# Kernel tuning notes

Measured on AMD Instinct MI355X. Metric: run time of the kernel, lower is better.

The kernel has to match this reference:

```python
import jax, jax.numpy as jnp
import numpy as np

DIM = 1024
NUM_HEADS = 16
HEAD_DIM = DIM // NUM_HEADS
SCALE = HEAD_DIM ** -0.5


def setup_inputs() -> dict:
    key = jax.random.key(0)
    ks = jax.random.split(key, 6)
    B, N, C = 2, 2048, DIM
    std = 1.0 / np.sqrt(C)
    x = jax.random.normal(ks[0], (B, N, C), dtype=jnp.float32)
    wq = jax.random.normal(ks[1], (C, C), dtype=jnp.float32) * std
    wk = jax.random.normal(ks[2], (C, C), dtype=jnp.float32) * std
    wv = jax.random.normal(ks[3], (C, C), dtype=jnp.float32) * std
    w_proj = jax.random.normal(ks[4], (C, C), dtype=jnp.float32) * std
    b_proj = jax.random.normal(ks[5], (C,), dtype=jnp.float32) * 0.01
    return {"x": x, "wq": wq, "wk": wk, "wv": wv, "w_proj": w_proj, "b_proj": b_proj}


def reference(x, wq, wk, wv, w_proj, b_proj):
    B, N, C = x.shape
    H, D = NUM_HEADS, HEAD_DIM
    Nq = N // 2
    # q from first half of tokens; k, v from all tokens
    q = (x[:, :Nq] @ wq.T).reshape(B, Nq, H, D).transpose(0, 2, 1, 3)  # [B,H,Nq,D]
    k = (x @ wk.T).reshape(B, N, H, D).transpose(0, 2, 1, 3)           # [B,H,N,D]
    v = (x @ wv.T).reshape(B, N, H, D).transpose(0, 2, 1, 3)           # [B,H,N,D]
    attn = jnp.einsum('bhqd,bhkd->bhqk', q, k) * SCALE
    attn = jax.nn.softmax(attn, axis=-1)
    out = jnp.einsum('bhqk,bhkd->bhqd', attn, v)                       # [B,H,Nq,D]
    out = out.transpose(0, 2, 1, 3).reshape(B, Nq, C)
    return out @ w_proj.T + b_proj
```

## Files before the change

### kernel.cpp

```cpp
#include <hip/hip_runtime.h>

typedef _Float16 f16;
typedef _Float16 f16x8 __attribute__((ext_vector_type(8)));
typedef _Float16 f16x4 __attribute__((ext_vector_type(4)));
typedef float f32x4 __attribute__((ext_vector_type(4)));

#define MFMA_F16(a, b, c) __builtin_amdgcn_mfma_f32_16x16x32_f16(a, b, c, 0, 0, 0)

__device__ __forceinline__ void gld16(const void* g, void* l) {
  __builtin_amdgcn_global_load_lds(
      (const __attribute__((address_space(1))) unsigned int*)(unsigned long long)g,
      (__attribute__((address_space(3))) unsigned int*)(unsigned long long)l, 16, 0, 0);
}

__global__ __launch_bounds__(256) void cvt_x_kernel(const float* __restrict__ in,
                                                    f16* __restrict__ out, int n8) {
  int i = blockIdx.x * 256 + threadIdx.x;
  if (i >= n8) return;
  const float4* p = (const float4*)(in + (size_t)i * 8);
  float4 a = p[0], b = p[1];
  f16x8 o = {(f16)a.x, (f16)a.y, (f16)a.z, (f16)a.w,
             (f16)b.x, (f16)b.y, (f16)b.z, (f16)b.w};
  *(f16x8*)(out + (size_t)i * 8) = o;
}

__global__ __launch_bounds__(256) void cvt_w4_kernel(const float* __restrict__ w0,
                                                     const float* __restrict__ w1,
                                                     const float* __restrict__ w2,
                                                     const float* __restrict__ w3,
                                                     f16* __restrict__ out) {
  int i = blockIdx.x * 256 + threadIdx.x;
  int t = i >> 17, r = i & 131071;
  const float* w = (t == 0) ? w0 : (t == 1) ? w1 : (t == 2) ? w2 : w3;
  const float4* p = (const float4*)(w + (size_t)r * 8);
  float4 a = p[0], b = p[1];
  f16x8 o = {(f16)a.x, (f16)a.y, (f16)a.z, (f16)a.w,
             (f16)b.x, (f16)b.y, (f16)b.z, (f16)b.w};
  *(f16x8*)(out + (size_t)t * 1048576 + (size_t)r * 8) = o;
}

__global__ __launch_bounds__(256) void qkv_gemm_kernel(
    const f16* __restrict__ A, const f16* __restrict__ Wq,
    const f16* __restrict__ Wk, const f16* __restrict__ Wv,
    f16* __restrict__ Qo, f16* __restrict__ Ko, f16* __restrict__ Vo) {
  __shared__ __align__(16) f16 As[128 * 64];
  __shared__ __align__(16) f16 Bs[128 * 64];
  const int y = blockIdx.y;
  const f16* Bw;
  f16* Co;
  int mt;
  if (y < 16) { Bw = Wq; Co = Qo; mt = (y & 7) | ((y >> 3) << 4); }
  else if (y < 48) { Bw = Wk; Co = Ko; mt = y - 16; }
  else { Bw = Wv; Co = Vo; mt = y - 48; }
  const int m0 = mt * 128, n0 = blockIdx.x * 128;
  const int tid = threadIdx.x, lane = tid & 63, w = tid >> 6;
  const int wr = w >> 1, wc = w & 1, g = lane >> 4, c = lane & 15;
  const int r_st = tid >> 3, t_st = tid & 7;

  f32x4 acc[4][4] = {};

  for (int k0 = 0; k0 < 1024; k0 += 64) {
#pragma unroll
    for (int i = 0; i < 4; ++i) {
      int row = r_st + i * 32;
      int sl = (t_st ^ (row & 7)) * 8;
      gld16(&A[(size_t)(m0 + row) * 1024 + k0 + sl], &As[(row * 8 + t_st) * 8]);
      gld16(&Bw[(size_t)(n0 + row) * 1024 + k0 + sl], &Bs[(row * 8 + t_st) * 8]);
    }
    __syncthreads();
#pragma unroll
    for (int kb = 0; kb < 2; ++kb) {
      f16x8 af[4], bf[4];
#pragma unroll
      for (int m2 = 0; m2 < 4; ++m2)
        af[m2] = *(const f16x8*)&As[(wr * 64 + m2 * 16 + c) * 64 +
                                    (((kb * 4 + g) ^ (c & 7)) * 8)];
#pragma unroll
      for (int nt = 0; nt < 4; ++nt)
        bf[nt] = *(const f16x8*)&Bs[(wc * 64 + nt * 16 + c) * 64 +
                                    (((kb * 4 + g) ^ (c & 7)) * 8)];
#pragma unroll
      for (int m2 = 0; m2 < 4; ++m2)
#pragma unroll
        for (int nt = 0; nt < 4; ++nt)
          acc[m2][nt] = MFMA_F16(af[m2], bf[nt], acc[m2][nt]);
    }
    __syncthreads();
  }

#pragma unroll
  for (int m2 = 0; m2 < 4; ++m2)
#pragma unroll
    for (int nt = 0; nt < 4; ++nt) {
      int col = n0 + wc * 64 + nt * 16 + c;
#pragma unroll
      for (int r = 0; r < 4; ++r)
        Co[(size_t)(m0 + wr * 64 + m2 * 16 + g * 4 + r) * 1024 + col] =
            (f16)acc[m2][nt][r];
    }
}

__global__ __launch_bounds__(256) void proj_gemm_kernel(
    const f16* __restrict__ A, const f16* __restrict__ Bw,
    float* __restrict__ C, const float* __restrict__ bias) {
  __shared__ __align__(16) f16 As[64 * 64];
  __shared__ __align__(16) f16 Bs[128 * 64];
  const int m0 = blockIdx.y * 64, n0 = blockIdx.x * 128;
  const int tid = threadIdx.x, lane = tid & 63, w = tid >> 6;
  const int wr = w >> 1, wc = w & 1, g = lane >> 4, c = lane & 15;
  const int r_st = tid >> 3, t_st = tid & 7;

  f32x4 acc[2][4] = {};

  for (int k0 = 0; k0 < 1024; k0 += 64) {
#pragma unroll
    for (int i = 0; i < 2; ++i) {
      int row = r_st + i * 32;
      int sl = (t_st ^ (row & 7)) * 8;
      gld16(&A[(size_t)(m0 + row) * 1024 + k0 + sl], &As[(row * 8 + t_st) * 8]);
    }
#pragma unroll
    for (int i = 0; i < 4; ++i) {
      int row = r_st + i * 32;
      int sl = (t_st ^ (row & 7)) * 8;
      gld16(&Bw[(size_t)(n0 + row) * 1024 + k0 + sl], &Bs[(row * 8 + t_st) * 8]);
    }
    __syncthreads();
#pragma unroll
    for (int kb = 0; kb < 2; ++kb) {
      f16x8 af[2], bf[4];
#pragma unroll
      for (int m2 = 0; m2 < 2; ++m2)
        af[m2] = *(const f16x8*)&As[(wr * 32 + m2 * 16 + c) * 64 +
                                    (((kb * 4 + g) ^ (c & 7)) * 8)];
#pragma unroll
      for (int nt = 0; nt < 4; ++nt)
        bf[nt] = *(const f16x8*)&Bs[(wc * 64 + nt * 16 + c) * 64 +
                                    (((kb * 4 + g) ^ (c & 7)) * 8)];
#pragma unroll
      for (int m2 = 0; m2 < 2; ++m2)
#pragma unroll
        for (int nt = 0; nt < 4; ++nt)
          acc[m2][nt] = MFMA_F16(af[m2], bf[nt], acc[m2][nt]);
    }
    __syncthreads();
  }

#pragma unroll
  for (int m2 = 0; m2 < 2; ++m2)
#pragma unroll
    for (int nt = 0; nt < 4; ++nt) {
      int col = n0 + wc * 64 + nt * 16 + c;
      float bv = bias[col];
#pragma unroll
      for (int r = 0; r < 4; ++r)
        C[(size_t)(m0 + wr * 32 + m2 * 16 + g * 4 + r) * 1024 + col] =
            acc[m2][nt][r] + bv;
    }
}

__global__ __launch_bounds__(256) void transpose_v_kernel(const f16* __restrict__ V,
                                                          f16* __restrict__ VT) {
  const int LDT = 72;
  __shared__ __align__(16) f16 T[64 * 72];
  const int n0 = blockIdx.x * 64, h = blockIdx.y, b = blockIdx.z;
  const int tid = threadIdx.x;
#pragma unroll
  for (int i = 0; i < 2; ++i) {
    int idx = tid + i * 256;
    int row = idx >> 3, c8 = idx & 7;
    *(f16x8*)&T[row * LDT + c8 * 8] =
        *(const f16x8*)&V[(size_t)(b * 2048 + n0 + row) * 1024 + h * 64 + c8 * 8];
  }
  __syncthreads();
#pragma unroll
  for (int i = 0; i < 2; ++i) {
    int idx = tid + i * 256;
    int d = idx >> 3, c8 = idx & 7;
    f16x8 v;
#pragma unroll
    for (int j = 0; j < 8; ++j) v[j] = T[(c8 * 8 + j) * LDT + d];
    *(f16x8*)&VT[((size_t)((b * 16 + h) * 64 + d)) * 2048 + n0 + c8 * 8] = v;
  }
}

__global__ __launch_bounds__(256, 4) void attn_kernel(const f16* __restrict__ Q,
                                                      const f16* __restrict__ Kg,
                                                      const f16* __restrict__ VT,
                                                      f16* __restrict__ Opart,
                                                      float2* __restrict__ ML) {
  __shared__ __align__(16) f16 Ks[2][64 * 64];
  __shared__ __align__(16) f16 Vs[2][64 * 64];
  __shared__ __align__(16) f16 Ps[4][16 * 64];
  const int qt = blockIdx.x, h = blockIdx.y;
  const int b = blockIdx.z >> 1, ch = blockIdx.z & 1;
  const int tid = threadIdx.x, lane = tid & 63, w = tid >> 6;
  const int g = lane >> 4, c = lane & 15;
  const int r_st = tid >> 3, t_st = tid & 7;

  const f16* Kbase = Kg + (size_t)(b * 2048 + ch * 1024) * 1024 + h * 64;
  const f16* Vbase = VT + ((size_t)((b * 16 + h) * 64)) * 2048 + ch * 1024;

  f16x8 qf[2];
  {
    const f16* qp = Q + (size_t)(b * 2048 + qt * 64 + w * 16 + c) * 1024 + h * 64;
    qf[0] = *(const f16x8*)(qp + g * 8);
    qf[1] = *(const f16x8*)(qp + 32 + g * 8);
#pragma unroll
    for (int j = 0; j < 8; ++j) {
      qf[0][j] = (f16)((float)qf[0][j] * 0.1803368801f);
      qf[1][j] = (f16)((float)qf[1][j] * 0.1803368801f);
    }
  }

  auto stage = [&](int t, int buf) {
#pragma unroll
    for (int i = 0; i < 2; ++i) {
      int row = r_st + i * 32;
      int sl = (t_st ^ (row & 7)) * 8;
      gld16(&Kbase[(size_t)(t * 64 + row) * 1024 + sl],
            &Ks[buf][(row * 8 + t_st) * 8]);
      gld16(&Vbase[(size_t)row * 2048 + t * 64 + sl],
            &Vs[buf][(row * 8 + t_st) * 8]);
    }
  };

  f32x4 oacc[4] = {};
  float l_run = 0.f;

  stage(0, 0);
  __syncthreads();

  for (int t = 0; t < 16; ++t) {
    const int cur = t & 1;
    if (t < 15) stage(t + 1, cur ^ 1);

    f32x4 s[4] = {};
#pragma unroll
    for (int kt = 0; kt < 4; ++kt) {
      f16x8 kf0 = *(const f16x8*)&Ks[cur][(kt * 16 + c) * 64 + ((g ^ (c & 7)) * 8)];
      f16x8 kf1 =
          *(const f16x8*)&Ks[cur][(kt * 16 + c) * 64 + (((4 + g) ^ (c & 7)) * 8)];
      s[kt] = MFMA_F16(kf0, qf[0], s[kt]);
      s[kt] = MFMA_F16(kf1, qf[1], s[kt]);
    }

    float rsum = 0.f;
#pragma unroll
    for (int kt = 0; kt < 4; ++kt)
#pragma unroll
      for (int r = 0; r < 4; ++r) {
        float p = exp2f(s[kt][r]);
        s[kt][r] = p;
        rsum += p;
      }
    rsum += __shfl_xor(rsum, 16);
    rsum += __shfl_xor(rsum, 32);
    l_run += rsum;

#pragma unroll
    for (int kt = 0; kt < 4; ++kt) {
      f16x4 pv = {(f16)s[kt][0], (f16)s[kt][1], (f16)s[kt][2], (f16)s[kt][3]};
      *(f16x4*)&Ps[w][c * 64 + (((kt * 2 + (g >> 1)) ^ (c & 7)) * 8) + (g & 1) * 4] =
          pv;
    }

#pragma unroll
    for (int kb = 0; kb < 2; ++kb) {
      f16x8 pf =
          *(const f16x8*)&Ps[w][c * 64 + (((kb * 4 + g) ^ (c & 7)) * 8)];
#pragma unroll
      for (int dt = 0; dt < 4; ++dt) {
        f16x8 vf = *(const f16x8*)&Vs[cur][(dt * 16 + c) * 64 +
                                           (((kb * 4 + g) ^ (c & 7)) * 8)];
        oacc[dt] = MFMA_F16(pf, vf, oacc[dt]);
      }
    }

    __syncthreads();
  }

  float li[4];
#pragma unroll
  for (int r = 0; r < 4; ++r) li[r] = 1.f / __shfl(l_run, g * 4 + r);
#pragma unroll
  for (int dt = 0; dt < 4; ++dt)
#pragma unroll
    for (int r = 0; r < 4; ++r) {
      Opart[(size_t)ch * 2097152 +
            (size_t)(b * 1024 + qt * 64 + w * 16 + g * 4 + r) * 1024 + h * 64 +
            dt * 16 + c] = (f16)(oacc[dt][r] * li[r]);
    }
  if (lane < 16)
    ML[ch * 32768 + (b * 1024 + qt * 64 + w * 16 + lane) * 16 + h] =
        make_float2(0.f, l_run);
}

__global__ __launch_bounds__(256) void combine_kernel(const f16* __restrict__ Opart,
                                                      const float2* __restrict__ ML,
                                                      f16* __restrict__ O16) {
  int i = blockIdx.x * 256 + threadIdx.x;
  int row = i >> 7;
  int h = (i & 127) >> 3;
  float2 a = ML[row * 16 + h];
  float2 bml = ML[32768 + row * 16 + h];
  float m = fmaxf(a.x, bml.x);
  float w0 = exp2f(a.x - m) * a.y;
  float w1 = exp2f(bml.x - m) * bml.y;
  float inv = 1.f / (w0 + w1);
  float a0 = w0 * inv, a1 = w1 * inv;
  f16x8 o0 = *(const f16x8*)&Opart[(size_t)i * 8];
  f16x8 o1 = *(const f16x8*)&Opart[2097152 + (size_t)i * 8];
  f16x8 r;
#pragma unroll
  for (int j = 0; j < 8; ++j) r[j] = (f16)(a0 * (float)o0[j] + a1 * (float)o1[j]);
  *(f16x8*)&O16[(size_t)i * 8] = r;
}

extern "C" void kernel_launch(void* const* d_in, const int* in_sizes, int n_in,
                              void* d_out, int out_size, void* d_ws, size_t ws_size,
                              hipStream_t stream) {
  const float* x = (const float*)d_in[0];
  const float* wq = (const float*)d_in[1];
  const float* wk = (const float*)d_in[2];
  const float* wv = (const float*)d_in[3];
  const float* wp = (const float*)d_in[4];
  const float* bp = (const float*)d_in[5];
  float* out = (float*)d_out;

  char* p = (char*)d_ws;
  f16* x16 = (f16*)p;  p += (size_t)4194304 * 2;
  f16* w16 = (f16*)p;  p += (size_t)4 * 1048576 * 2;
  f16* Q16 = (f16*)p;  p += (size_t)4194304 * 2;
  f16* K16 = (f16*)p;  p += (size_t)4194304 * 2;
  f16* V16 = (f16*)p;  p += (size_t)4194304 * 2;
  f16* VT16 = (f16*)p; p += (size_t)4194304 * 2;
  f16* O16 = (f16*)p;  p += (size_t)2097152 * 2;

  f16* wq16 = w16;
  f16* wk16 = w16 + 1048576;
  f16* wv16 = w16 + 2 * 1048576;
  f16* wp16 = w16 + 3 * 1048576;

  cvt_x_kernel<<<4194304 / 8 / 256, 256, 0, stream>>>(x, x16, 4194304 / 8);
  cvt_w4_kernel<<<4 * 131072 / 256, 256, 0, stream>>>(wq, wk, wv, wp, w16);

  qkv_gemm_kernel<<<dim3(8, 80), 256, 0, stream>>>(x16, wq16, wk16, wv16, Q16, K16,
                                                   V16);

  transpose_v_kernel<<<dim3(32, 16, 2), 256, 0, stream>>>(V16, VT16);

  f16* Opart = V16;
  float2* MLp = (float2*)x16;
  attn_kernel<<<dim3(16, 16, 4), 256, 0, stream>>>(Q16, K16, VT16, Opart, MLp);
  combine_kernel<<<1024, 256, 0, stream>>>(Opart, MLp, O16);

  proj_gemm_kernel<<<dim3(8, 32), 256, 0, stream>>>(O16, wp16, out, bp);
}
```

Baseline: 114.5 us.

## Double-buffer GEMMs, fuse V transpose into QKV epilogue, swizzle block order

The QKV and projection GEMMs now double-buffer their shared-memory tiles, issuing the next k-tile's async global-to-LDS loads before computing on the current one. The QKV epilogue writes V directly in transposed layout, so the separate transpose kernel and its extra round trip through global memory are removed. Block indices in the GEMMs and the attention kernel are remapped with an XCD-style swizzle to improve L2 locality across chiplets. The projection GEMM moves to 64x64 tiles with twice as many blocks, and LDS use per block doubles in the QKV GEMM, which may lower occupancy.

```diff
diff --git a/kernel.cpp b/kernel.cpp
--- a/kernel.cpp
+++ b/kernel.cpp
@@ -42,43 +42,52 @@
 __global__ __launch_bounds__(256) void qkv_gemm_kernel(
     const f16* __restrict__ A, const f16* __restrict__ Wq,
     const f16* __restrict__ Wk, const f16* __restrict__ Wv,
-    f16* __restrict__ Qo, f16* __restrict__ Ko, f16* __restrict__ Vo) {
-  __shared__ __align__(16) f16 As[128 * 64];
-  __shared__ __align__(16) f16 Bs[128 * 64];
-  const int y = blockIdx.y;
+    f16* __restrict__ Qo, f16* __restrict__ Ko, f16* __restrict__ VT) {
+  __shared__ __align__(16) f16 As[2][128 * 64];
+  __shared__ __align__(16) f16 Bs[2][128 * 64];
+  const int bid = blockIdx.x + blockIdx.y * 8;
+  const int swz = (bid & 7) * 80 + (bid >> 3);
+  const int bx = swz & 7, y = swz >> 3;
   const f16* Bw;
-  f16* Co;
-  int mt;
+  f16* Co = nullptr;
+  int mt, isv = 0;
   if (y < 16) { Bw = Wq; Co = Qo; mt = (y & 7) | ((y >> 3) << 4); }
   else if (y < 48) { Bw = Wk; Co = Ko; mt = y - 16; }
-  else { Bw = Wv; Co = Vo; mt = y - 48; }
-  const int m0 = mt * 128, n0 = blockIdx.x * 128;
+  else { Bw = Wv; isv = 1; mt = y - 48; }
+  const int m0 = mt * 128, n0 = bx * 128;
   const int tid = threadIdx.x, lane = tid & 63, w = tid >> 6;
   const int wr = w >> 1, wc = w & 1, g = lane >> 4, c = lane & 15;
   const int r_st = tid >> 3, t_st = tid & 7;
 
-  f32x4 acc[4][4] = {};
-
-  for (int k0 = 0; k0 < 1024; k0 += 64) {
+  auto stage = [&](int k0, int buf) {
 #pragma unroll
     for (int i = 0; i < 4; ++i) {
       int row = r_st + i * 32;
       int sl = (t_st ^ (row & 7)) * 8;
-      gld16(&A[(size_t)(m0 + row) * 1024 + k0 + sl], &As[(row * 8 + t_st) * 8]);
-      gld16(&Bw[(size_t)(n0 + row) * 1024 + k0 + sl], &Bs[(row * 8 + t_st) * 8]);
-    }
-    __syncthreads();
+      gld16(&A[(size_t)(m0 + row) * 1024 + k0 + sl], &As[buf][(row * 8 + t_st) * 8]);
+      gld16(&Bw[(size_t)(n0 + row) * 1024 + k0 + sl], &Bs[buf][(row * 8 + t_st) * 8]);
+    }
+  };
+
+  f32x4 acc[4][4] = {};
+
+  stage(0, 0);
+  __syncthreads();
+
+  for (int t = 0; t < 16; ++t) {
+    const int cur = t & 1;
+    if (t < 15) stage((t + 1) * 64, cur ^ 1);
 #pragma unroll
     for (int kb = 0; kb < 2; ++kb) {
       f16x8 af[4], bf[4];
 #pragma unroll
       for (int m2 = 0; m2 < 4; ++m2)
-        af[m2] = *(const f16x8*)&As[(wr * 64 + m2 * 16 + c) * 64 +
-                                    (((kb * 4 + g) ^ (c & 7)) * 8)];
+        af[m2] = *(const f16x8*)&As[cur][(wr * 64 + m2 * 16 + c) * 64 +
+                                         (((kb * 4 + g) ^ (c & 7)) * 8)];
 #pragma unroll
       for (int nt = 0; nt < 4; ++nt)
-        bf[nt] = *(const f16x8*)&Bs[(wc * 64 + nt * 16 + c) * 64 +
-                                    (((kb * 4 + g) ^ (c & 7)) * 8)];
+        bf[nt] = *(const f16x8*)&Bs[cur][(wc * 64 + nt * 16 + c) * 64 +
+                                         (((kb * 4 + g) ^ (c & 7)) * 8)];
 #pragma unroll
       for (int m2 = 0; m2 < 4; ++m2)
 #pragma unroll
@@ -88,100 +97,94 @@
     __syncthreads();
   }
 
-#pragma unroll
-  for (int m2 = 0; m2 < 4; ++m2)
-#pragma unroll
-    for (int nt = 0; nt < 4; ++nt) {
-      int col = n0 + wc * 64 + nt * 16 + c;
-#pragma unroll
-      for (int r = 0; r < 4; ++r)
-        Co[(size_t)(m0 + wr * 64 + m2 * 16 + g * 4 + r) * 1024 + col] =
-            (f16)acc[m2][nt][r];
-    }
+  if (isv) {
+    const int b = m0 >> 11;
+    const int n_base = (m0 & 2047) + wr * 64 + g * 4;
+#pragma unroll
+    for (int m2 = 0; m2 < 4; ++m2)
+#pragma unroll
+      for (int nt = 0; nt < 4; ++nt) {
+        int col = n0 + wc * 64 + nt * 16 + c;
+        int h = col >> 6, d = col & 63;
+        f16x4 pv = {(f16)acc[m2][nt][0], (f16)acc[m2][nt][1],
+                    (f16)acc[m2][nt][2], (f16)acc[m2][nt][3]};
+        *(f16x4*)&VT[((size_t)((b * 16 + h) * 64 + d)) * 2048 + n_base + m2 * 16] = pv;
+      }
+  } else {
+#pragma unroll
+    for (int m2 = 0; m2 < 4; ++m2)
+#pragma unroll
+      for (int nt = 0; nt < 4; ++nt) {
+        int col = n0 + wc * 64 + nt * 16 + c;
+#pragma unroll
+        for (int r = 0; r < 4; ++r)
+          Co[(size_t)(m0 + wr * 64 + m2 * 16 + g * 4 + r) * 1024 + col] =
+              (f16)acc[m2][nt][r];
+      }
+  }
 }
 
 __global__ __launch_bounds__(256) void proj_gemm_kernel(
     const f16* __restrict__ A, const f16* __restrict__ Bw,
     float* __restrict__ C, const float* __restrict__ bias) {
-  __shared__ __align__(16) f16 As[64 * 64];
-  __shared__ __align__(16) f16 Bs[128 * 64];
-  const int m0 = blockIdx.y * 64, n0 = blockIdx.x * 128;
+  __shared__ __align__(16) f16 As[2][64 * 64];
+  __shared__ __align__(16) f16 Bs[2][64 * 64];
+  const int bid = blockIdx.x + blockIdx.y * 16;
+  const int swz = (bid & 7) * 64 + (bid >> 3);
+  const int m0 = (swz >> 4) * 64, n0 = (swz & 15) * 64;
   const int tid = threadIdx.x, lane = tid & 63, w = tid >> 6;
   const int wr = w >> 1, wc = w & 1, g = lane >> 4, c = lane & 15;
   const int r_st = tid >> 3, t_st = tid & 7;
 
-  f32x4 acc[2][4] = {};
-
-  for (int k0 = 0; k0 < 1024; k0 += 64) {
+  auto stage = [&](int k0, int buf) {
 #pragma unroll
     for (int i = 0; i < 2; ++i) {
       int row = r_st + i * 32;
       int sl = (t_st ^ (row & 7)) * 8;
-      gld16(&A[(size_t)(m0 + row) * 1024 + k0 + sl], &As[(row * 8 + t_st) * 8]);
-    }
-#pragma unroll
-    for (int i = 0; i < 4; ++i) {
-      int row = r_st + i * 32;
-      int sl = (t_st ^ (row & 7)) * 8;
-      gld16(&Bw[(size_t)(n0 + row) * 1024 + k0 + sl], &Bs[(row * 8 + t_st) * 8]);
+      gld16(&A[(size_t)(m0 + row) * 1024 + k0 + sl], &As[buf][(row * 8 + t_st) * 8]);
+      gld16(&Bw[(size_t)(n0 + row) * 1024 + k0 + sl], &Bs[buf][(row * 8 + t_st) * 8]);
+    }
+  };
+
+  f32x4 acc[2][2] = {};
+
+  stage(0, 0);
+  __syncthreads();
+
+  for (int t = 0; t < 16; ++t) {
+    const int cur = t & 1;
+    if (t < 15) stage((t + 1) * 64, cur ^ 1);
+#pragma unroll
+    for (int kb = 0; kb < 2; ++kb) {
+      f16x8 af[2], bf[2];
+#pragma unroll
+      for (int m2 = 0; m2 < 2; ++m2)
+        af[m2] = *(const f16x8*)&As[cur][(wr * 32 + m2 * 16 + c) * 64 +
+                                         (((kb * 4 + g) ^ (c & 7)) * 8)];
+#pragma unroll
+      for (int nt = 0; nt < 2; ++nt)
+        bf[nt] = *(const f16x8*)&Bs[cur][(wc * 32 + nt * 16 + c) * 64 +
+                                         (((kb * 4 + g) ^ (c & 7)) * 8)];
+#pragma unroll
+      for (int m2 = 0; m2 < 2; ++m2)
+#pragma unroll
+        for (int nt = 0; nt < 2; ++nt)
+          acc[m2][nt] = MFMA_F16(af[m2], bf[nt], acc[m2][nt]);
     }
     __syncthreads();
-#pragma unroll
-    for (int kb = 0; kb < 2; ++kb) {
-      f16x8 af[2], bf[4];
-#pragma unroll
-      for (int m2 = 0; m2 < 2; ++m2)
-        af[m2] = *(const f16x8*)&As[(wr * 32 + m2 * 16 + c) * 64 +
-                                    (((kb * 4 + g) ^ (c & 7)) * 8)];
-#pragma unroll
-      for (int nt = 0; nt < 4; ++nt)
-        bf[nt] = *(const f16x8*)&Bs[(wc * 64 + nt * 16 + c) * 64 +
-                                    (((kb * 4 + g) ^ (c & 7)) * 8)];
-#pragma unroll
-      for (int m2 = 0; m2 < 2; ++m2)
-#pragma unroll
-        for (int nt = 0; nt < 4; ++nt)
-          acc[m2][nt] = MFMA_F16(af[m2], bf[nt], acc[m2][nt]);
-    }
-    __syncthreads();
   }
 
 #pragma unroll
   for (int m2 = 0; m2 < 2; ++m2)
 #pragma unroll
-    for (int nt = 0; nt < 4; ++nt) {
-      int col = n0 + wc * 64 + nt * 16 + c;
+    for (int nt = 0; nt < 2; ++nt) {
+      int col = n0 + wc * 32 + nt * 16 + c;
       float bv = bias[col];
 #pragma unroll
       for (int r = 0; r < 4; ++r)
         C[(size_t)(m0 + wr * 32 + m2 * 16 + g * 4 + r) * 1024 + col] =
             acc[m2][nt][r] + bv;
     }
-}
-
-__global__ __launch_bounds__(256) void transpose_v_kernel(const f16* __restrict__ V,
-                                                          f16* __restrict__ VT) {
-  const int LDT = 72;
-  __shared__ __align__(16) f16 T[64 * 72];
-  const int n0 = blockIdx.x * 64, h = blockIdx.y, b = blockIdx.z;
-  const int tid = threadIdx.x;
-#pragma unroll
-  for (int i = 0; i < 2; ++i) {
-    int idx = tid + i * 256;
-    int row = idx >> 3, c8 = idx & 7;
-    *(f16x8*)&T[row * LDT + c8 * 8] =
-        *(const f16x8*)&V[(size_t)(b * 2048 + n0 + row) * 1024 + h * 64 + c8 * 8];
-  }
-  __syncthreads();
-#pragma unroll
-  for (int i = 0; i < 2; ++i) {
-    int idx = tid + i * 256;
-    int d = idx >> 3, c8 = idx & 7;
-    f16x8 v;
-#pragma unroll
-    for (int j = 0; j < 8; ++j) v[j] = T[(c8 * 8 + j) * LDT + d];
-    *(f16x8*)&VT[((size_t)((b * 16 + h) * 64 + d)) * 2048 + n0 + c8 * 8] = v;
-  }
 }
 
 __global__ __launch_bounds__(256, 4) void attn_kernel(const f16* __restrict__ Q,
@@ -192,8 +195,10 @@
   __shared__ __align__(16) f16 Ks[2][64 * 64];
   __shared__ __align__(16) f16 Vs[2][64 * 64];
   __shared__ __align__(16) f16 Ps[4][16 * 64];
-  const int qt = blockIdx.x, h = blockIdx.y;
-  const int b = blockIdx.z >> 1, ch = blockIdx.z & 1;
+  const int flat = blockIdx.x + blockIdx.y * 16 + blockIdx.z * 256;
+  const int swz = (flat & 7) * 128 + (flat >> 3);
+  const int qt = swz & 15, h = (swz >> 4) & 15;
+  const int b = (swz >> 9) & 1, ch = (swz >> 8) & 1;
   const int tid = threadIdx.x, lane = tid & 63, w = tid >> 6;
   const int g = lane >> 4, c = lane & 15;
   const int r_st = tid >> 3, t_st = tid & 7;
@@ -267,8 +272,7 @@
 
 #pragma unroll
     for (int kb = 0; kb < 2; ++kb) {
-      f16x8 pf =
-          *(const f16x8*)&Ps[w][c * 64 + (((kb * 4 + g) ^ (c & 7)) * 8)];
+      f16x8 pf = *(const f16x8*)&Ps[w][c * 64 + (((kb * 4 + g) ^ (c & 7)) * 8)];
 #pragma unroll
       for (int dt = 0; dt < 4; ++dt) {
         f16x8 vf = *(const f16x8*)&Vs[cur][(dt * 16 + c) * 64 +
@@ -333,7 +337,7 @@
   f16* w16 = (f16*)p;  p += (size_t)4 * 1048576 * 2;
   f16* Q16 = (f16*)p;  p += (size_t)4194304 * 2;
   f16* K16 = (f16*)p;  p += (size_t)4194304 * 2;
-  f16* V16 = (f16*)p;  p += (size_t)4194304 * 2;
+  f16* Opart = (f16*)p; p += (size_t)4194304 * 2;
   f16* VT16 = (f16*)p; p += (size_t)4194304 * 2;
   f16* O16 = (f16*)p;  p += (size_t)2097152 * 2;
 
@@ -346,14 +350,11 @@
   cvt_w4_kernel<<<4 * 131072 / 256, 256, 0, stream>>>(wq, wk, wv, wp, w16);
 
   qkv_gemm_kernel<<<dim3(8, 80), 256, 0, stream>>>(x16, wq16, wk16, wv16, Q16, K16,
-                                                   V16);
-
-  transpose_v_kernel<<<dim3(32, 16, 2), 256, 0, stream>>>(V16, VT16);
-
-  f16* Opart = V16;
+                                                   VT16);
+
   float2* MLp = (float2*)x16;
   attn_kernel<<<dim3(16, 16, 4), 256, 0, stream>>>(Q16, K16, VT16, Opart, MLp);
   combine_kernel<<<1024, 256, 0, stream>>>(Opart, MLp, O16);
 
-  proj_gemm_kernel<<<dim3(8, 32), 256, 0, stream>>>(O16, wp16, out, bp);
-}
+  proj_gemm_kernel<<<dim3(16, 32), 256, 0, stream>>>(O16, wp16, out, bp);
+}
```

Measured after the change: 96.30 us. 1.19x faster.
